# Kernel optimization log

Measured on AMD Instinct MI355X. Metric: run time of the kernel, lower is better.

Reference implementation:

```python
import jax, jax.numpy as jnp
import numpy as np

B, S, D = 4, 4096, 1024
DD = 4 * D
N_EXPERTS = 8
CAPACITY = 1.0
LN_EPS = 1e-5


def setup_inputs() -> dict:
    key = jax.random.key(0)
    ks = jax.random.split(key, 8)
    s1 = 1.0 / np.sqrt(D)
    s2 = 1.0 / np.sqrt(DD)
    return {
        "x": jax.random.normal(ks[0], (B, S, D), jnp.float32),
        "gate_w": jax.random.normal(ks[1], (N_EXPERTS, D), jnp.float32) * 0.02,
        "ln_w": jnp.ones((D,), jnp.float32),
        "ln_b": jnp.zeros((D,), jnp.float32),
        "fc1s": jax.random.normal(ks[2], (N_EXPERTS, DD, D), jnp.float32) * s1,
        "b1s": jax.random.normal(ks[3], (N_EXPERTS, DD), jnp.float32) * s1,
        "fc2s": jax.random.normal(ks[4], (N_EXPERTS, D, DD), jnp.float32) * s2,
        "b2s": jax.random.normal(ks[5], (N_EXPERTS, D), jnp.float32) * s2,
    }


def reference(x, gate_w, ln_w, ln_b, fc1s, b1s, fc2s, b2s):
    og_shape = x.shape
    d = og_shape[-1]
    xf = x.reshape(-1, d)                       # (bs, d)
    bs = xf.shape[0]
    n = gate_w.shape[0]
    k = int(bs * CAPACITY) // n                 # static capacity per expert

    # softmax gating over experts
    scores = jax.nn.softmax(xf @ gate_w.T, axis=-1)   # (bs, n)

    # per-expert top-k tokens (column-wise descending sort, take first k)
    vals, idx = jax.lax.top_k(scores.T, k)      # (n, k)
    kept_w = vals.T                              # (k, n)
    kept_idx = idx.T                             # (k, n)
    flat_idx = kept_idx.reshape(-1)              # (k*n,) row-major: k outer, n inner

    # gather selected tokens, layernorm
    y = xf[flat_idx].reshape(k, n, d)            # (k, n, d)
    mu = y.mean(-1, keepdims=True)
    var = ((y - mu) ** 2).mean(-1, keepdims=True)
    y = (y - mu) * jax.lax.rsqrt(var + LN_EPS) * ln_w + ln_b

    # per-expert grouped GEMMs
    h = jnp.einsum('knd,nfd->knf', y, fc1s) + b1s          # (k, n, dd)
    h = jax.nn.gelu(h, approximate=True)                   # tanh gelu
    out = jnp.einsum('knf,ndf->knd', h, fc2s) + b2s        # (k, n, d)

    # weight by gate scores and scatter-add back onto the input tokens
    out = out * kept_w[..., None]
    xf = xf.at[flat_idx].add(out.reshape(k * n, d))
    return xf.reshape(og_shape)
```

## Files before the change

kernel.cpp:

```cpp
#include <hip/hip_runtime.h>

#define TOK  16384
#define NEXP 8
#define DIM  1024
#define DDIM 4096
#define KCAP 2048

typedef float  floatx4 __attribute__((ext_vector_type(4)));
typedef short  shortx8 __attribute__((ext_vector_type(8)));

static __device__ __forceinline__ unsigned short f2bf(float x) {
  unsigned u = __float_as_uint(x);
  return (unsigned short)((u + 0x7fffu + ((u >> 16) & 1u)) >> 16);
}

__global__ __launch_bounds__(256) void cvt_kernel(const float* __restrict__ src,
                                                  unsigned short* __restrict__ dst, int n4) {
  int i = blockIdx.x * 256 + threadIdx.x;
  if (i < n4) {
    float4 v = ((const float4*)src)[i];
    ushort4 o = make_ushort4(f2bf(v.x), f2bf(v.y), f2bf(v.z), f2bf(v.w));
    ((ushort4*)dst)[i] = o;
  }
}

__global__ __launch_bounds__(256) void gate_kernel(const float* __restrict__ x,
                                                   const float* __restrict__ gw,
                                                   float* __restrict__ scores) {
  __shared__ float gws[NEXP * DIM];
  int tid = threadIdx.x;
  for (int i = tid; i < NEXP * DIM / 4; i += 256)
    ((float4*)gws)[i] = ((const float4*)gw)[i];
  __syncthreads();
  int wave = tid >> 6, lane = tid & 63;
  int t = blockIdx.x * 4 + wave;
  const float4* xr = (const float4*)(x + (size_t)t * DIM);
  float4 xv[4];
#pragma unroll
  for (int j = 0; j < 4; ++j) xv[j] = xr[j * 64 + lane];
  float acc[NEXP];
#pragma unroll
  for (int e = 0; e < NEXP; ++e) acc[e] = 0.f;
#pragma unroll
  for (int e = 0; e < NEXP; ++e) {
    const float4* g4 = (const float4*)(gws + e * DIM);
#pragma unroll
    for (int j = 0; j < 4; ++j) {
      float4 g = g4[j * 64 + lane];
      acc[e] += xv[j].x * g.x + xv[j].y * g.y + xv[j].z * g.z + xv[j].w * g.w;
    }
  }
#pragma unroll
  for (int off = 32; off > 0; off >>= 1) {
#pragma unroll
    for (int e = 0; e < NEXP; ++e) acc[e] += __shfl_down(acc[e], off);
  }
  if (lane == 0) {
    float mx = acc[0];
#pragma unroll
    for (int e = 1; e < NEXP; ++e) mx = fmaxf(mx, acc[e]);
    float ex[NEXP], sum = 0.f;
#pragma unroll
    for (int e = 0; e < NEXP; ++e) { ex[e] = expf(acc[e] - mx); sum += ex[e]; }
    float inv = 1.f / sum;
#pragma unroll
    for (int e = 0; e < NEXP; ++e) scores[(size_t)e * TOK + t] = ex[e] * inv;
  }
}

#define TKT 1024
#define TKW (TKT / 64)
__global__ __launch_bounds__(TKT) void topk_kernel(const float* __restrict__ scores,
                                                   int* __restrict__ sel,
                                                   float* __restrict__ selw) {
  int e = blockIdx.x;
  const float* s = scores + (size_t)e * TOK;
  int tid = threadIdx.x, lane = tid & 63, wave = tid >> 6;
  __shared__ int cnt;
  __shared__ int wsum[TKW];

  unsigned prefix = 0;
  for (int bit = 30; bit >= 0; --bit) {
    unsigned cand = prefix | (1u << bit);
    if (tid == 0) cnt = 0;
    __syncthreads();
    int c = 0;
    for (int i = tid; i < TOK; i += TKT) c += (__float_as_uint(s[i]) >= cand) ? 1 : 0;
#pragma unroll
    for (int off = 32; off > 0; off >>= 1) c += __shfl_down(c, off);
    if (lane == 0) atomicAdd(&cnt, c);
    __syncthreads();
    if (cnt >= KCAP) prefix = cand;
    __syncthreads();
  }
  unsigned T = prefix;

  if (tid == 0) cnt = 0;
  __syncthreads();
  {
    int c = 0;
    for (int i = tid; i < TOK; i += TKT) c += (__float_as_uint(s[i]) > T) ? 1 : 0;
#pragma unroll
    for (int off = 32; off > 0; off >>= 1) c += __shfl_down(c, off);
    if (lane == 0) atomicAdd(&cnt, c);
  }
  __syncthreads();
  int n_gt = cnt;
  int need = KCAP - n_gt;

  __shared__ int pos;
  __shared__ int tiebase;
  if (tid == 0) { pos = 0; tiebase = 0; }
  __syncthreads();
  for (int chunk = 0; chunk < TOK; chunk += TKT) {
    int i = chunk + tid;
    unsigned v = __float_as_uint(s[i]);
    if (v > T) {
      int p = atomicAdd(&pos, 1);
      sel[e * KCAP + p]  = i;
      selw[e * KCAP + p] = __uint_as_float(v);
    }
    bool tie = (v == T);
    unsigned long long m = __ballot(tie);
    if (lane == 0) wsum[wave] = __popcll(m);
    __syncthreads();
    int base = tiebase;
    for (int w = 0; w < wave; ++w) base += wsum[w];
    int rank = base + __popcll(m & ((1ull << lane) - 1ull));
    if (tie && rank < need) {
      sel[e * KCAP + n_gt + rank]  = i;
      selw[e * KCAP + n_gt + rank] = __uint_as_float(T);
    }
    __syncthreads();
    if (tid == 0) {
      int tb = 0;
#pragma unroll
      for (int w = 0; w < TKW; ++w) tb += wsum[w];
      tiebase += tb;
    }
    __syncthreads();
  }
}

__global__ __launch_bounds__(256) void gather_ln_kernel(const float* __restrict__ x,
                                                        const int* __restrict__ sel,
                                                        const float* __restrict__ lnw,
                                                        const float* __restrict__ lnb,
                                                        unsigned short* __restrict__ Y) {
  int e = blockIdx.y, i = blockIdx.x;
  int tid = threadIdx.x, lane = tid & 63, wave = tid >> 6;
  int t = sel[e * KCAP + i];
  const float4* xr = (const float4*)(x + (size_t)t * DIM);
  float4 v = xr[tid];
  float s  = v.x + v.y + v.z + v.w;
  float sq = v.x * v.x + v.y * v.y + v.z * v.z + v.w * v.w;
#pragma unroll
  for (int off = 32; off > 0; off >>= 1) { s += __shfl_down(s, off); sq += __shfl_down(sq, off); }
  __shared__ float red[8];
  if (lane == 0) { red[wave] = s; red[4 + wave] = sq; }
  __syncthreads();
  s  = red[0] + red[1] + red[2] + red[3];
  sq = red[4] + red[5] + red[6] + red[7];
  float mu  = s * (1.f / DIM);
  float var = sq * (1.f / DIM) - mu * mu;
  float rs  = rsqrtf(var + 1e-5f);
  float4 w = ((const float4*)lnw)[tid];
  float4 b = ((const float4*)lnb)[tid];
  ushort4 o = make_ushort4(f2bf((v.x - mu) * rs * w.x + b.x),
                           f2bf((v.y - mu) * rs * w.y + b.y),
                           f2bf((v.z - mu) * rs * w.z + b.z),
                           f2bf((v.w - mu) * rs * w.w + b.w));
  ((ushort4*)(Y + ((size_t)e * KCAP + i) * DIM))[tid] = o;
}

#define BM  128
#define BN  128
#define BKT 64

template <int MODE>
__global__ __launch_bounds__(256) void gemm_kernel(
    const unsigned short* __restrict__ Aall,
    const unsigned short* __restrict__ Ball,
    const float* __restrict__ biasAll,
    int M, int N, int K,
    unsigned short* __restrict__ Hall,
    float* __restrict__ Out,
    const int* __restrict__ sel, const float* __restrict__ selw) {
  int e = blockIdx.z;
  const unsigned short* A = Aall + (size_t)e * M * K;
  const unsigned short* B = Ball + (size_t)e * N * K;
  const float* bias = biasAll + (size_t)e * N;

  __shared__ __align__(16) unsigned short As[BM * BKT];
  __shared__ __align__(16) unsigned short Bs[BN * BKT];
  __shared__ int   selS[BM];
  __shared__ float wS[BM];

  int tid = threadIdx.x, lane = tid & 63, wave = tid >> 6;
  int m0 = blockIdx.y * BM, n0 = blockIdx.x * BN;
  if (MODE == 2 && tid < BM) {
    selS[tid] = sel[e * KCAP + m0 + tid];
    wS[tid]   = selw[e * KCAP + m0 + tid];
  }
  int wm = (wave & 1) * 64, wn = (wave >> 1) * 64;
  int r8 = lane >> 3;
  int j8 = lane & 7;
  int scol = (j8 ^ r8) * 8;
  int row = lane & 15, quad = lane >> 4;
  int r7 = row & 7;

  floatx4 acc[4][4];
  floatx4 zero = {0.f, 0.f, 0.f, 0.f};
#pragma unroll
  for (int a = 0; a < 4; ++a)
#pragma unroll
    for (int b = 0; b < 4; ++b) acc[a][b] = zero;

  for (int k0 = 0; k0 < K; k0 += BKT) {
    __syncthreads();
#pragma unroll
    for (int j = 0; j < 4; ++j) {
      int q = wave * 4 + j;
      const unsigned short* ga = A + (size_t)(m0 + q * 8 + r8) * K + k0 + scol;
      __builtin_amdgcn_global_load_lds((const __attribute__((address_space(1))) void*)ga,
                                       (__attribute__((address_space(3))) void*)(As + q * 512),
                                       16, 0, 0);
      const unsigned short* gb = B + (size_t)(n0 + q * 8 + r8) * K + k0 + scol;
      __builtin_amdgcn_global_load_lds((const __attribute__((address_space(1))) void*)gb,
                                       (__attribute__((address_space(3))) void*)(Bs + q * 512),
                                       16, 0, 0);
    }
    __syncthreads();
#pragma unroll
    for (int kk = 0; kk < BKT; kk += 32) {
      int xg = ((quad + (kk >> 3)) ^ r7) << 3;
      shortx8 af[4], bf[4];
#pragma unroll
      for (int ti = 0; ti < 4; ++ti)
        af[ti] = *(const shortx8*)&As[(wm + ti * 16 + row) * BKT + xg];
#pragma unroll
      for (int tj = 0; tj < 4; ++tj)
        bf[tj] = *(const shortx8*)&Bs[(wn + tj * 16 + row) * BKT + xg];
#pragma unroll
      for (int ti = 0; ti < 4; ++ti)
#pragma unroll
        for (int tj = 0; tj < 4; ++tj)
          acc[ti][tj] = __builtin_amdgcn_mfma_f32_16x16x32_bf16(af[ti], bf[tj], acc[ti][tj], 0, 0, 0);
    }
  }

#pragma unroll
  for (int ti = 0; ti < 4; ++ti) {
#pragma unroll
    for (int tj = 0; tj < 4; ++tj) {
      int gn = n0 + wn + tj * 16 + row;
      float bb = bias[gn];
#pragma unroll
      for (int r = 0; r < 4; ++r) {
        int lrow = wm + ti * 16 + quad * 4 + r;
        float v = acc[ti][tj][r] + bb;
        if (MODE == 1) {
          float u = 0.7978845608028654f * (v + 0.044715f * v * v * v);
          u = fminf(u, 15.f);
          float e2 = __expf(2.f * u);
          float th = __fdividef(e2 - 1.f, e2 + 1.f);
          float g = 0.5f * v * (1.f + th);
          Hall[(size_t)e * M * N + (size_t)(m0 + lrow) * N + gn] = f2bf(g);
        } else {
          atomicAdd(&Out[(size_t)selS[lrow] * DIM + gn], wS[lrow] * v);
        }
      }
    }
  }
}

extern "C" void kernel_launch(void* const* d_in, const int* in_sizes, int n_in,
                              void* d_out, int out_size, void* d_ws, size_t ws_size,
                              hipStream_t stream) {
  const float* x   = (const float*)d_in[0];
  const float* gw  = (const float*)d_in[1];
  const float* lnw = (const float*)d_in[2];
  const float* lnb = (const float*)d_in[3];
  const float* fc1 = (const float*)d_in[4];
  const float* b1  = (const float*)d_in[5];
  const float* fc2 = (const float*)d_in[6];
  const float* b2  = (const float*)d_in[7];
  float* out = (float*)d_out;

  char* p = (char*)d_ws;
  float* scores = (float*)p;                 p += (size_t)NEXP * TOK * 4;
  int*   sel    = (int*)p;                   p += (size_t)NEXP * KCAP * 4;
  float* selw   = (float*)p;                 p += (size_t)NEXP * KCAP * 4;
  unsigned short* Wb = (unsigned short*)p;   p += (size_t)NEXP * DDIM * DIM * 2;
  unsigned short* Y  = (unsigned short*)p;   p += (size_t)NEXP * KCAP * DIM * 2;
  unsigned short* H  = (unsigned short*)p;   p += (size_t)NEXP * KCAP * DDIM * 2;

  hipMemcpyAsync(out, x, (size_t)TOK * DIM * sizeof(float), hipMemcpyDeviceToDevice, stream);

  gate_kernel<<<TOK / 4, 256, 0, stream>>>(x, gw, scores);
  topk_kernel<<<NEXP, TKT, 0, stream>>>(scores, sel, selw);
  gather_ln_kernel<<<dim3(KCAP, NEXP), 256, 0, stream>>>(x, sel, lnw, lnb, Y);

  const int n4w = NEXP * DDIM * DIM / 4;
  cvt_kernel<<<n4w / 256, 256, 0, stream>>>(fc1, Wb, n4w);
  gemm_kernel<1><<<dim3(DDIM / BN, KCAP / BM, NEXP), 256, 0, stream>>>(
      Y, Wb, b1, KCAP, DDIM, DIM, H, nullptr, nullptr, nullptr);

  cvt_kernel<<<n4w / 256, 256, 0, stream>>>(fc2, Wb, n4w);
  gemm_kernel<2><<<dim3(DIM / BN, KCAP / BM, NEXP), 256, 0, stream>>>(
      H, Wb, b2, KCAP, DIM, DDIM, nullptr, out, sel, selw);
}
```

Before: 908.6 us.

## Rewrite expert GEMM as 256x256 double-buffered, phase-interleaved MFMA kernel

Replaces the 128x128 single-buffered GEMM with a 256x256 tile over 512 threads (8 waves). The kernel double-buffers LDS and interleaves async global-to-LDS loads of the next K-step with four MFMA phases, using s_setprio and explicit waitcnt/barriers. It also flattens the grid into a 1D launch with an XCD-aware block swizzle. The aim is to hide global load latency, raise data reuse per tile and improve L2 locality. In exchange it uses far more LDS and registers, and the hand-written waitcnt accounting is fragile.

```diff
diff --git a/kernel.cpp b/kernel.cpp
--- a/kernel.cpp
+++ b/kernel.cpp
@@ -173,12 +173,13 @@
   ((ushort4*)(Y + ((size_t)e * KCAP + i) * DIM))[tid] = o;
 }
 
-#define BM  128
-#define BN  128
+#define BM  256
+#define BN  256
 #define BKT 64
+#define HTILE 8192
 
 template <int MODE>
-__global__ __launch_bounds__(256) void gemm_kernel(
+__global__ __launch_bounds__(512, 2) void gemm_kernel(
     const unsigned short* __restrict__ Aall,
     const unsigned short* __restrict__ Ball,
     const float* __restrict__ biasAll,
@@ -186,78 +187,128 @@
     unsigned short* __restrict__ Hall,
     float* __restrict__ Out,
     const int* __restrict__ sel, const float* __restrict__ selw) {
-  int e = blockIdx.z;
+
+  __shared__ __align__(16) unsigned short As[2 * 2 * HTILE];
+  __shared__ __align__(16) unsigned short Bs[2 * 2 * HTILE];
+  __shared__ int   selS[BM];
+  __shared__ float wS[BM];
+
+  int tid = threadIdx.x, lane = tid & 63, wave = tid >> 6;
+  int m_w = wave >> 2, n_w = wave & 3;
+  int hb  = n_w >> 1, nb0 = (n_w & 1) * 64;
+  int row = lane & 15, quad = lane >> 4, r7 = row & 7;
+  int r8 = lane >> 3, j8 = lane & 7;
+
+  int nxt = N >> 8, nyt = M >> 8, per = nxt * nyt;
+  int nwg = per * NEXP;
+  int bid = blockIdx.x;
+  int swz = (bid & 7) * (nwg >> 3) + (bid >> 3);
+  int e   = swz / per;
+  int rem = swz - e * per;
+  int by  = rem / nxt;
+  int bx  = rem - by * nxt;
+  int m0 = by * BM, n0 = bx * BN;
+  int NT = K / BKT;
+
   const unsigned short* A = Aall + (size_t)e * M * K;
   const unsigned short* B = Ball + (size_t)e * N * K;
   const float* bias = biasAll + (size_t)e * N;
 
-  __shared__ __align__(16) unsigned short As[BM * BKT];
-  __shared__ __align__(16) unsigned short Bs[BN * BKT];
-  __shared__ int   selS[BM];
-  __shared__ float wS[BM];
-
-  int tid = threadIdx.x, lane = tid & 63, wave = tid >> 6;
-  int m0 = blockIdx.y * BM, n0 = blockIdx.x * BN;
   if (MODE == 2 && tid < BM) {
     selS[tid] = sel[e * KCAP + m0 + tid];
     wS[tid]   = selw[e * KCAP + m0 + tid];
   }
-  int wm = (wave & 1) * 64, wn = (wave >> 1) * 64;
-  int r8 = lane >> 3;
-  int j8 = lane & 7;
-  int scol = (j8 ^ r8) * 8;
-  int row = lane & 15, quad = lane >> 4;
-  int r7 = row & 7;
-
-  floatx4 acc[4][4];
+  __syncthreads();
+
+#define STAGE(DST, G, RC0, TT, HALF, BUF)                                              \
+  do {                                                                                 \
+    int tt_ = (TT) < NT ? (TT) : NT - 1;                                               \
+    const unsigned short* g_ =                                                         \
+        (G) + (size_t)((RC0) + (HALF) * 128 + wave * 16 + r8) * K + tt_ * BKT +        \
+        ((j8 ^ r8) << 3);                                                              \
+    unsigned short* l_ = (DST) + ((BUF) * 2 + (HALF)) * HTILE + wave * 16 * 64;        \
+    __builtin_amdgcn_global_load_lds((const __attribute__((address_space(1))) void*)g_,\
+        (__attribute__((address_space(3))) void*)l_, 16, 0, 0);                        \
+    __builtin_amdgcn_global_load_lds(                                                  \
+        (const __attribute__((address_space(1))) void*)(g_ + (size_t)8 * K),           \
+        (__attribute__((address_space(3))) void*)(l_ + 8 * 64), 16, 0, 0);             \
+  } while (0)
+
+#define LDA(MQ)                                                                        \
+  _Pragma("unroll") for (int ti = 0; ti < 4; ++ti)                                     \
+  _Pragma("unroll") for (int kki = 0; kki < 2; ++kki)                                  \
+    a[ti][kki] = *(const shortx8*)&As[(cur * 2 + m_w) * HTILE +                        \
+        ((MQ) * 64 + ti * 16 + row) * 64 + (((quad + 4 * kki) ^ r7) << 3)];
+
+#define LDB(BREG, NQ)                                                                  \
+  _Pragma("unroll") for (int tj = 0; tj < 2; ++tj)                                     \
+  _Pragma("unroll") for (int kki = 0; kki < 2; ++kki)                                  \
+    BREG[tj][kki] = *(const shortx8*)&Bs[(cur * 2 + hb) * HTILE +                      \
+        (nb0 + (NQ) * 32 + tj * 16 + row) * 64 + (((quad + 4 * kki) ^ r7) << 3)];
+
+#define MFMAQ(MQ, BREG, NQ)                                                            \
+  _Pragma("unroll") for (int ti = 0; ti < 4; ++ti)                                     \
+  _Pragma("unroll") for (int tj = 0; tj < 2; ++tj)                                     \
+  _Pragma("unroll") for (int kki = 0; kki < 2; ++kki)                                  \
+    acc[(MQ) * 4 + ti][(NQ) * 2 + tj] = __builtin_amdgcn_mfma_f32_16x16x32_bf16(       \
+        a[ti][kki], BREG[tj][kki], acc[(MQ) * 4 + ti][(NQ) * 2 + tj], 0, 0, 0);
+
+#define PH_MID()                                                                       \
+  __builtin_amdgcn_s_barrier();                                                        \
+  asm volatile("s_waitcnt lgkmcnt(0)" ::: "memory");                                   \
+  __builtin_amdgcn_s_setprio(1);
+
+#define PH_END()                                                                       \
+  __builtin_amdgcn_s_setprio(0);                                                       \
+  __builtin_amdgcn_s_barrier();
+
+#define PH_END_VM()                                                                    \
+  __builtin_amdgcn_s_setprio(0);                                                       \
+  asm volatile("s_waitcnt vmcnt(2)" ::: "memory");                                     \
+  __builtin_amdgcn_s_barrier();
+
+  floatx4 acc[8][4];
   floatx4 zero = {0.f, 0.f, 0.f, 0.f};
 #pragma unroll
-  for (int a = 0; a < 4; ++a)
-#pragma unroll
-    for (int b = 0; b < 4; ++b) acc[a][b] = zero;
-
-  for (int k0 = 0; k0 < K; k0 += BKT) {
-    __syncthreads();
-#pragma unroll
-    for (int j = 0; j < 4; ++j) {
-      int q = wave * 4 + j;
-      const unsigned short* ga = A + (size_t)(m0 + q * 8 + r8) * K + k0 + scol;
-      __builtin_amdgcn_global_load_lds((const __attribute__((address_space(1))) void*)ga,
-                                       (__attribute__((address_space(3))) void*)(As + q * 512),
-                                       16, 0, 0);
-      const unsigned short* gb = B + (size_t)(n0 + q * 8 + r8) * K + k0 + scol;
-      __builtin_amdgcn_global_load_lds((const __attribute__((address_space(1))) void*)gb,
-                                       (__attribute__((address_space(3))) void*)(Bs + q * 512),
-                                       16, 0, 0);
-    }
-    __syncthreads();
-#pragma unroll
-    for (int kk = 0; kk < BKT; kk += 32) {
-      int xg = ((quad + (kk >> 3)) ^ r7) << 3;
-      shortx8 af[4], bf[4];
-#pragma unroll
-      for (int ti = 0; ti < 4; ++ti)
-        af[ti] = *(const shortx8*)&As[(wm + ti * 16 + row) * BKT + xg];
-#pragma unroll
-      for (int tj = 0; tj < 4; ++tj)
-        bf[tj] = *(const shortx8*)&Bs[(wn + tj * 16 + row) * BKT + xg];
-#pragma unroll
-      for (int ti = 0; ti < 4; ++ti)
-#pragma unroll
-        for (int tj = 0; tj < 4; ++tj)
-          acc[ti][tj] = __builtin_amdgcn_mfma_f32_16x16x32_bf16(af[ti], bf[tj], acc[ti][tj], 0, 0, 0);
-    }
-  }
-
-#pragma unroll
-  for (int ti = 0; ti < 4; ++ti) {
+  for (int i = 0; i < 8; ++i)
+#pragma unroll
+    for (int j = 0; j < 4; ++j) acc[i][j] = zero;
+
+  shortx8 a[4][2], b0[2][2], b1[2][2];
+
+  STAGE(As, A, m0, 0, 0, 0);
+  STAGE(As, A, m0, 0, 1, 0);
+  STAGE(Bs, B, n0, 0, 0, 0);
+  STAGE(Bs, B, n0, 0, 1, 0);
+  STAGE(As, A, m0, 1, 0, 1);
+  asm volatile("s_waitcnt vmcnt(2)" ::: "memory");
+  __builtin_amdgcn_s_barrier();
+
+  for (int t = 0; t < NT; ++t) {
+    int cur = t & 1, nb = cur ^ 1;
+    LDA(0); LDB(b0, 0);
+    STAGE(As, A, m0, t + 1, 1, nb);
+    asm volatile("s_waitcnt lgkmcnt(8)" ::: "memory");
+    PH_MID(); MFMAQ(0, b0, 0); PH_END();
+    LDB(b1, 1);
+    STAGE(Bs, B, n0, t + 1, 0, nb);
+    PH_MID(); MFMAQ(0, b1, 1); PH_END();
+    LDA(1);
+    STAGE(Bs, B, n0, t + 1, 1, nb);
+    PH_MID(); MFMAQ(1, b0, 0); PH_END();
+    STAGE(As, A, m0, t + 2, 0, cur);
+    PH_MID(); MFMAQ(1, b1, 1); PH_END_VM();
+  }
+
+#pragma unroll
+  for (int ti = 0; ti < 8; ++ti) {
 #pragma unroll
     for (int tj = 0; tj < 4; ++tj) {
-      int gn = n0 + wn + tj * 16 + row;
+      int gn = n0 + n_w * 64 + tj * 16 + row;
       float bb = bias[gn];
 #pragma unroll
       for (int r = 0; r < 4; ++r) {
-        int lrow = wm + ti * 16 + quad * 4 + r;
+        int lrow = m_w * 128 + ti * 16 + quad * 4 + r;
         float v = acc[ti][tj][r] + bb;
         if (MODE == 1) {
           float u = 0.7978845608028654f * (v + 0.044715f * v * v * v);
@@ -272,6 +323,13 @@
       }
     }
   }
+#undef STAGE
+#undef LDA
+#undef LDB
+#undef MFMAQ
+#undef PH_MID
+#undef PH_END
+#undef PH_END_VM
 }
 
 extern "C" void kernel_launch(void* const* d_in, const int* in_sizes, int n_in,
@@ -303,10 +361,10 @@
 
   const int n4w = NEXP * DDIM * DIM / 4;
   cvt_kernel<<<n4w / 256, 256, 0, stream>>>(fc1, Wb, n4w);
-  gemm_kernel<1><<<dim3(DDIM / BN, KCAP / BM, NEXP), 256, 0, stream>>>(
+  gemm_kernel<1><<<dim3((DDIM / BN) * (KCAP / BM) * NEXP), 512, 0, stream>>>(
       Y, Wb, b1, KCAP, DDIM, DIM, H, nullptr, nullptr, nullptr);
 
   cvt_kernel<<<n4w / 256, 256, 0, stream>>>(fc2, Wb, n4w);
-  gemm_kernel<2><<<dim3(DIM / BN, KCAP / BM, NEXP), 256, 0, stream>>>(
+  gemm_kernel<2><<<dim3((DIM / BN) * (KCAP / BM) * NEXP), 512, 0, stream>>>(
       H, Wb, b2, KCAP, DIM, DDIM, nullptr, out, sel, selw);
 }
```

Measured after the change: 780.2 us. 14.1% less time.
